# Kernel optimization log

Hardware: AMD Instinct MI355X
Metric: run time of the kernel (lower is better)

## Reference

```python
import jax, jax.numpy as jnp
import numpy as np

B, T, D, L, VOCAB = 4, 2048, 512, 3, 256


def setup_inputs() -> dict:
    key = jax.random.key(0)
    ks = jax.random.split(key, 5)
    x = jax.random.randint(ks[0], (B, T), 0, VOCAB, dtype=jnp.int32)
    embed = jax.random.normal(ks[1], (VOCAB, D), dtype=jnp.float32) * 0.02
    k = jnp.ones((L,), dtype=jnp.float32)
    ln_gamma = jnp.ones((L, D), dtype=jnp.float32)
    ln_beta = jnp.zeros((L, D), dtype=jnp.float32)
    W1 = jax.random.normal(ks[2], (L, D, 4 * D), dtype=jnp.float32) * 0.02
    b1 = jnp.zeros((L, 4 * D), dtype=jnp.float32)
    W2 = jax.random.normal(ks[3], (L, 4 * D, D), dtype=jnp.float32) * 0.02
    b2 = jnp.zeros((L, D), dtype=jnp.float32)
    return {"x": x, "embed": embed, "k": k, "ln_gamma": ln_gamma,
            "ln_beta": ln_beta, "W1": W1, "b1": b1, "W2": W2, "b2": b2}


def _layernorm(x, g, b, eps=1e-3):  # keras default eps=1e-3
    mu = jnp.mean(x, axis=-1, keepdims=True)
    var = jnp.mean(jnp.square(x - mu), axis=-1, keepdims=True)
    return (x - mu) * jax.lax.rsqrt(var + eps) * g + b


def reference(x, embed, k, ln_gamma, ln_beta, W1, b1, W2, b2):
    h = embed[x]  # (B,T,D)
    # CumprodBoundaryDimension: cumprod over feature dim, tanh, cumsum over time
    bd = jnp.cumsum(jnp.tanh(jnp.cumprod(h, axis=-1)), axis=1)
    h = h + h * bd
    t = jnp.arange(T)
    dist = jnp.abs((t[:, None] - t[None, :]).astype(jnp.float32))  # (T,T)
    causal = (t[None, :] <= t[:, None]).astype(jnp.float32)
    for l in range(L):
        # DeltaImportance
        h_cum = jnp.cumsum(h, axis=1)
        h_prev = jnp.pad(h[:, :-1, :], ((0, 0), (1, 0), (0, 0)))
        mag = jnp.linalg.norm(h_cum - h_prev, axis=-1)  # (B,T)
        decay = jnp.exp(-jax.nn.softplus(k[l]) * dist) * causal  # (T,T)
        # importance[b,i,j] = mag[b,i]*decay[i,j]; context = importance @ h
        ctx = jnp.abs(mag[:, :, None] * jnp.einsum('ij,bjd->bid', decay, h))
        y = _layernorm(ctx, ln_gamma[l], ln_beta[l])
        y = jax.nn.gelu(y @ W1[l] + b1[l], approximate=False) @ W2[l] + b2[l]
        h = h + y
    return h @ embed.T  # tied output projection (B,T,VOCAB)
```

## Files before the change

### kernel.cpp

```cpp
#include <hip/hip_runtime.h>
#include <math.h>


constexpr int Bc = 4, Tc = 2048, Dc = 512, Hc = 2048, Vc = 256;
constexpr int TSF = 16, NCF = 128, WARM = 20;

typedef __attribute__((ext_vector_type(8))) short short8;
typedef __attribute__((ext_vector_type(4))) float f32x4;

__device__ inline unsigned short f2bf(float f) {
  unsigned int u = __float_as_uint(f);
  u += 0x7fffu + ((u >> 16) & 1u);
  return (unsigned short)(u >> 16);
}

__device__ inline void gload_lds16(const void* g, void* l) {
  __builtin_amdgcn_global_load_lds(
      (const __attribute__((address_space(1))) void*)g,
      (__attribute__((address_space(3))) void*)l, 16, 0, 0);
}

__device__ inline float gelu_f(float z) {
  float x = z * 0.707106781186547524f;
  float ax = fabsf(x);
  float t = 1.0f / (1.0f + 0.3275911f * ax);
  float poly = t*(0.254829592f + t*(-0.284496736f + t*(1.421413741f +
               t*(-1.453152027f + t*1.061405429f))));
  float er = 1.0f - poly * __expf(-ax*ax);
  er = copysignf(er, x);
  return 0.5f * z * (1.0f + er);
}

__device__ inline void tr32(const float* Wl, unsigned short* Wtl,
                            int R, int C, int c0, int r0, int tid,
                            float (*tile)[33]) {
  int tx = tid & 31, ty = tid >> 5;
  for (int i = ty; i < 32; i += 8)
    tile[i][tx] = Wl[(size_t)(r0+i)*C + (c0+tx)];
  __syncthreads();
  for (int i = ty; i < 32; i += 8)
    Wtl[(size_t)(c0+i)*R + (r0+tx)] = f2bf(tile[tx][i]);
}

__global__ __launch_bounds__(256) void wprep(
    const float* __restrict__ W1, unsigned short* __restrict__ W1t,
    const float* __restrict__ W2, unsigned short* __restrict__ W2t,
    const float* __restrict__ embed, unsigned short* __restrict__ emb)
{
  __shared__ float tile[32][33];
  int bid = blockIdx.x, tid = threadIdx.x;
  if (bid < 3072) {
    int l = bid >> 10, rem = bid & 1023;
    int cx = rem & 63, ry = rem >> 6;
    tr32(W1 + (size_t)l*Dc*Hc, W1t + (size_t)l*Dc*Hc, Dc, Hc,
         cx*32, ry*32, tid, tile);
  } else if (bid < 6144) {
    int b2 = bid - 3072;
    int l = b2 >> 10, rem = b2 & 1023;
    int cx = rem & 15, ry = rem >> 4;
    tr32(W2 + (size_t)l*Hc*Dc, W2t + (size_t)l*Hc*Dc, Hc, Dc,
         cx*32, ry*32, tid, tile);
  } else {
    int i = (bid - 6144)*256 + tid;
    if (i < Vc*Dc) emb[i] = f2bf(embed[i]);
  }
}

__global__ __launch_bounds__(1024) void embed_part(
    const int* __restrict__ x, const float* __restrict__ embed,
    float* __restrict__ th, float* __restrict__ partA)
{
  int c = blockIdx.x, b = blockIdx.y;
  int wv = threadIdx.x >> 6, lane = threadIdx.x & 63;
  int token = b*Tc + c*TSF + wv;
  int row = x[token];
  const float* e = embed + (size_t)row * Dc + lane * 8;
  float v[8];
  {
    float4 a = *(const float4*)e;
    float4 bb = *(const float4*)(e + 4);
    v[0]=a.x; v[1]=a.y; v[2]=a.z; v[3]=a.w;
    v[4]=bb.x; v[5]=bb.y; v[6]=bb.z; v[7]=bb.w;
  }
  float p = v[0];
  #pragma unroll
  for (int j=1;j<8;++j) p *= v[j];
  float incl = p;
  #pragma unroll
  for (int off=1; off<64; off<<=1) {
    float t = __shfl_up(incl, off);
    if (lane >= off) incl *= t;
  }
  float excl = __shfl_up(incl, 1);
  if (lane == 0) excl = 1.0f;
  float cc = excl;
  float o[8];
  #pragma unroll
  for (int j=0;j<8;++j) { cc *= v[j]; o[j] = tanhf(cc); }
  float* dst = th + (size_t)token * Dc + lane * 8;
  *(float4*)dst     = make_float4(o[0],o[1],o[2],o[3]);
  *(float4*)(dst+4) = make_float4(o[4],o[5],o[6],o[7]);
  __syncthreads();
  int d = threadIdx.x;
  if (d < Dc) {
    const float* pp = th + ((size_t)b*Tc + c*TSF)*Dc + d;
    float s = 0.f;
    #pragma unroll
    for (int t=0;t<TSF;++t) s += pp[(size_t)t*Dc];
    partA[((size_t)b*NCF + c)*Dc + d] = s;
  }
}

__global__ __launch_bounds__(512) void part_prefix(float* __restrict__ part)
{
  int pair = blockIdx.x * 8 + (threadIdx.x >> 6);
  int lane = threadIdx.x & 63;
  int b = pair >> 9, d = pair & 511;
  size_t i0 = ((size_t)b*NCF + 2*lane)*Dc + d;
  float v0 = part[i0];
  float v1 = part[i0 + Dc];
  float ps = v0 + v1;
  float incl = ps;
  #pragma unroll
  for (int off=1; off<64; off<<=1) {
    float t = __shfl_up(incl, off);
    if (lane >= off) incl += t;
  }
  float excl = incl - ps;
  part[i0]      = excl;
  part[i0 + Dc] = excl + v0;
}

__global__ __launch_bounds__(512) void bd_apply(
    const float* __restrict__ th, const float* __restrict__ partA,
    const int* __restrict__ x, const float* __restrict__ embed,
    float* __restrict__ h, float* __restrict__ partB)
{
  int c = blockIdx.x, b = blockIdx.y, d = threadIdx.x;
  float acc = partA[((size_t)b*NCF + c)*Dc + d];
  float hsum = 0.f;
  #pragma unroll
  for (int t=0;t<TSF;++t) {
    int tt = c*TSF + t;
    size_t idx = ((size_t)b*Tc + tt)*Dc + d;
    acc += th[idx];
    int row = x[b*Tc + tt];
    float e = embed[(size_t)row*Dc + d];
    float hv = e * (1.0f + acc);
    h[idx] = hv;
    hsum += hv;
  }
  partB[((size_t)b*NCF + c)*Dc + d] = hsum;
}

__global__ __launch_bounds__(512) void mag_scan_ln(
    const float* __restrict__ h, const float* __restrict__ part,
    const float* __restrict__ kvec, int l,
    const float* __restrict__ g, const float* __restrict__ bt,
    unsigned short* __restrict__ yb)
{
  __shared__ float redA[8][TSF];
  __shared__ float redB[8][TSF];
  __shared__ float mag[TSF], muS[TSF], rsS[TSF];
  int c = blockIdx.x, b = blockIdx.y, d = threadIdx.x;
  int lane = d & 63, wv = d >> 6;
  float acc = part[((size_t)b*NCF + c)*Dc + d];
  int t0 = c * TSF;
  const float* hbase = h + (size_t)b*Tc*Dc + d;
  float hp = (t0 > 0) ? hbase[(size_t)(t0-1)*Dc] : 0.f;
  float hv[TSF];
  #pragma unroll
  for (int t=0;t<TSF;++t) {
    hv[t] = hbase[(size_t)(t0+t)*Dc];
    acc += hv[t];
    float diff = acc - hp;
    hp = hv[t];
    float s = diff * diff;
    #pragma unroll
    for (int off=32; off; off>>=1) s += __shfl_down(s, off);
    if (!lane) redA[wv][t] = s;
  }
  float kk = kvec[l];
  float sp = kk > 0.f ? kk + log1pf(expf(-kk)) : log1pf(expf(kk));
  float w = expf(-sp);
  int ts = t0 - WARM; if (ts < 0) ts = 0;
  float s = 0.f;
  for (int t=ts; t<t0; ++t) s = hbase[(size_t)t*Dc] + w*s;
  __syncthreads();
  if (d < TSF) {
    float m = 0.f;
    #pragma unroll
    for (int w2=0;w2<8;++w2) m += redA[w2][d];
    mag[d] = sqrtf(m);
  }
  __syncthreads();
  #pragma unroll
  for (int t=0;t<TSF;++t) {
    s = hv[t] + w * s;
    float cv = mag[t] * fabsf(s);
    hv[t] = cv;
    float s1 = cv, s2 = cv * cv;
    #pragma unroll
    for (int off=32; off; off>>=1) {
      s1 += __shfl_down(s1, off);
      s2 += __shfl_down(s2, off);
    }
    if (!lane) { redA[wv][t] = s1; redB[wv][t] = s2; }
  }
  __syncthreads();
  if (d < TSF) {
    float m1 = 0.f, m2 = 0.f;
    #pragma unroll
    for (int w2=0;w2<8;++w2) { m1 += redA[w2][d]; m2 += redB[w2][d]; }
    float mu = m1 * (1.f/Dc);
    float var = fmaxf(m2 * (1.f/Dc) - mu*mu, 0.f);
    muS[d] = mu;
    rsS[d] = rsqrtf(var + 1e-3f);
  }
  __syncthreads();
  float gv = g[l*Dc + d], bv = bt[l*Dc + d];
  unsigned short* yp = yb + ((size_t)b*Tc + t0)*Dc + d;
  #pragma unroll
  for (int t=0;t<TSF;++t)
    yp[(size_t)t*Dc] = f2bf((hv[t] - muS[t]) * rsS[t] * gv + bv);
}

template<int CH> __device__ inline int swz(int row) {
  if constexpr (CH == 8) return row & 7;
  else return (row & 3) ^ ((row >> 3) & 1);
}

template<int EPI, int TM, int TN, int BK>
__global__ __launch_bounds__(256) void mgemm(
    const unsigned short* __restrict__ A,
    const unsigned short* __restrict__ Bt,
    const float* __restrict__ bias,
    float* __restrict__ C, unsigned short* __restrict__ Cb,
    float* __restrict__ part,
    int N, int K, int nrow)
{
  constexpr int CH = BK / 8;
  constexpr int PA = TM*CH/256, PB = TN*CH/256;
  constexpr int WM = TM/2, WN = TN/2;
  constexpr int AM = WM/16, AN = WN/16;
  constexpr int NKH = BK/32;
  constexpr int ASTG = TM*BK, BSTG = TN*BK;
  __shared__ unsigned short As[2*ASTG];
  __shared__ unsigned short Bs[2*BSTG];
  int tid = threadIdx.x;
  int lane = tid & 63, w = tid >> 6;
  int wr = w >> 1, wc = w & 1;
  int bid = blockIdx.x;
  int xcd = bid & 7, i = bid >> 3;
  int npx = nrow >> 3;
  int m0 = (xcd * npx + (i % npx)) * TM;
  int n0 = (i / npx) * TN;

  const unsigned short* ag[PA];
  const unsigned short* bg[PB];
  int aldst[PA], bldst[PB];
  #pragma unroll
  for (int p=0;p<PA;++p) {
    int ci = p*256 + tid;
    int row = ci / CH, cp = ci % CH;
    int cg = cp ^ swz<CH>(row);
    ag[p] = A + (size_t)(m0+row)*K + cg*8;
    aldst[p] = (p*256 + w*64)*8;
  }
  #pragma unroll
  for (int p=0;p<PB;++p) {
    int ci = p*256 + tid;
    int row = ci / CH, cp = ci % CH;
    int cg = cp ^ swz<CH>(row);
    bg[p] = Bt + (size_t)(n0+row)*K + cg*8;
    bldst[p] = (p*256 + w*64)*8;
  }

  int r = lane & 15, quad = lane >> 4;
  int aoff[NKH][AM], boff[NKH][AN];
  #pragma unroll
  for (int kh=0;kh<NKH;++kh) {
    int cb = kh*4 + quad;
    #pragma unroll
    for (int i2=0;i2<AM;++i2)
      aoff[kh][i2] = (wr*WM + i2*16 + r)*BK + ((cb ^ swz<CH>(r)) & (CH-1))*8;
    #pragma unroll
    for (int j=0;j<AN;++j)
      boff[kh][j] = (wc*WN + j*16 + r)*BK + ((cb ^ swz<CH>(r)) & (CH-1))*8;
  }

  f32x4 acc[AM][AN];
  #pragma unroll
  for (int i2=0;i2<AM;++i2)
    #pragma unroll
    for (int j=0;j<AN;++j)
      acc[i2][j] = (f32x4){0.f,0.f,0.f,0.f};

  #pragma unroll
  for (int p=0;p<PA;++p) gload_lds16(ag[p], &As[aldst[p]]);
  #pragma unroll
  for (int p=0;p<PB;++p) gload_lds16(bg[p], &Bs[bldst[p]]);

  int nk = K / BK;
  for (int ki = 0; ki < nk; ++ki) {
    __syncthreads();
    int cur = ki & 1, nxt = cur ^ 1;
    if (ki + 1 < nk) {
      int kk = (ki + 1) * BK;
      #pragma unroll
      for (int p=0;p<PA;++p) gload_lds16(ag[p] + kk, &As[nxt*ASTG + aldst[p]]);
      #pragma unroll
      for (int p=0;p<PB;++p) gload_lds16(bg[p] + kk, &Bs[nxt*BSTG + bldst[p]]);
    }
    #pragma unroll
    for (int kh=0;kh<NKH;++kh) {
      short8 af[AM], bfr[AN];
      #pragma unroll
      for (int i2=0;i2<AM;++i2) af[i2] = *(const short8*)&As[cur*ASTG + aoff[kh][i2]];
      #pragma unroll
      for (int j=0;j<AN;++j) bfr[j] = *(const short8*)&Bs[cur*BSTG + boff[kh][j]];
      #pragma unroll
      for (int i2=0;i2<AM;++i2)
        #pragma unroll
        for (int j=0;j<AN;++j)
          acc[i2][j] = __builtin_amdgcn_mfma_f32_16x16x32_bf16(af[i2], bfr[j], acc[i2][j], 0, 0, 0);
    }
  }

  #pragma unroll
  for (int i2=0;i2<AM;++i2) {
    int rowb = m0 + wr*WM + i2*16 + quad*4;
    #pragma unroll
    for (int j=0;j<AN;++j) {
      int col = n0 + wc*WN + j*16 + r;
      float bv = 0.f;
      if (EPI != 2) bv = bias[col];
      float ps = 0.f;
      #pragma unroll
      for (int reg=0;reg<4;++reg) {
        size_t idx = (size_t)(rowb + reg) * N + col;
        float z = acc[i2][j][reg] + bv;
        if (EPI == 0) {
          Cb[idx] = f2bf(gelu_f(z));
        } else if (EPI == 1) {
          float hv = C[idx] + z;
          C[idx] = hv;
          ps += hv;
          if (Cb) Cb[idx] = f2bf(hv);
        } else {
          C[idx] = z;
        }
      }
      if (EPI == 1 && part) {
        ps += __shfl_xor(ps, 16);
        ps += __shfl_xor(ps, 32);
        if (quad == 0) {
          int chunk = (m0 + wr*WM + i2*16) >> 4;
          part[(size_t)chunk * N + col] = ps;
        }
      }
    }
  }
}

extern "C" void kernel_launch(void* const* d_in, const int* in_sizes, int n_in,
                              void* d_out, int out_size, void* d_ws, size_t ws_size,
                              hipStream_t stream) {
  const int*   x     = (const int*)  d_in[0];
  const float* embed = (const float*)d_in[1];
  const float* kvec  = (const float*)d_in[2];
  const float* g     = (const float*)d_in[3];
  const float* bt    = (const float*)d_in[4];
  const float* W1    = (const float*)d_in[5];
  const float* b1    = (const float*)d_in[6];
  const float* W2    = (const float*)d_in[7];
  const float* b2    = (const float*)d_in[8];
  float* out = (float*)d_out;

  const size_t NTD = (size_t)Bc * Tc * Dc;
  const size_t NTH = (size_t)Bc * Tc * Hc;
  char* wsb = (char*)d_ws;
  float* h      = (float*)wsb;                wsb += NTD*4;
  float* tmpA   = (float*)wsb;                wsb += NTD*4;
  float* partA  = (float*)wsb;                wsb += (size_t)Bc*NCF*Dc*4;
  float* partB  = (float*)wsb;                wsb += (size_t)Bc*NCF*Dc*4;
  unsigned short* yb   = (unsigned short*)wsb; wsb += NTD*2;
  unsigned short* a1b  = (unsigned short*)wsb; wsb += NTH*2;
  unsigned short* hb   = (unsigned short*)wsb; wsb += NTD*2;
  unsigned short* W1t  = (unsigned short*)wsb; wsb += (size_t)3*Dc*Hc*2;
  unsigned short* W2t  = (unsigned short*)wsb; wsb += (size_t)3*Dc*Hc*2;
  unsigned short* emb  = (unsigned short*)wsb; wsb += (size_t)Vc*Dc*2;

  wprep<<<dim3(6144 + (Vc*Dc+255)/256), 256, 0, stream>>>(
      W1, W1t, W2, W2t, embed, emb);

  embed_part<<<dim3(NCF, Bc), 1024, 0, stream>>>(x, embed, tmpA, partA);
  part_prefix<<<dim3(256), 512, 0, stream>>>(partA);
  bd_apply<<<dim3(NCF, Bc), 512, 0, stream>>>(tmpA, partA, x, embed, h, partB);
  part_prefix<<<dim3(256), 512, 0, stream>>>(partB);

  for (int l = 0; l < 3; ++l) {
    mag_scan_ln<<<dim3(NCF, Bc), 512, 0, stream>>>(h, partB, kvec, l, g, bt, yb);
    mgemm<0,64,64,64><<<dim3(128*(Hc/64)), 256, 0, stream>>>(
        yb, W1t + (size_t)l*Hc*Dc, b1 + (size_t)l*Hc, nullptr, a1b, nullptr,
        Hc, Dc, 128);
    mgemm<1,64,64,64><<<dim3(128*(Dc/64)), 256, 0, stream>>>(
        a1b, W2t + (size_t)l*Dc*Hc, b2 + (size_t)l*Dc, h,
        (l == 2) ? hb : nullptr, (l < 2) ? partB : nullptr, Dc, Hc, 128);
    if (l < 2) part_prefix<<<dim3(256), 512, 0, stream>>>(partB);
  }
  mgemm<2,64,64,32><<<dim3(128*(Vc/64)), 256, 0, stream>>>(
      hb, emb, nullptr, out, nullptr, nullptr, Vc, Dc, 128);
}
```

Before: 407.5 us.

## Fuse prologue scans and mag/LN into cooperative kernels with grid syncs

Merges the embedding cumprod/tanh, both chunk-prefix scans, the boundary apply and the first-layer mag-scan/layernorm into one cooperative kernel that uses grid-wide syncs. It also folds the per-layer part_prefix into the following mag-scan kernel. The tanh intermediate stays in shared memory instead of a global tmp buffer. This removes several kernel launches and a full-size global round trip, at the cost of cooperative launch overhead and grid barrier latency, and it needs all 512 blocks to be co-resident.

```diff
diff --git a/kernel.cpp b/kernel.cpp
--- a/kernel.cpp
+++ b/kernel.cpp
@@ -1,6 +1,9 @@
 #include <hip/hip_runtime.h>
+#include <hip/hip_cooperative_groups.h>
 #include <math.h>
 
+
+namespace cg = cooperative_groups;
 
 constexpr int Bc = 4, Tc = 2048, Dc = 512, Hc = 2048, Vc = 256;
 constexpr int TSF = 16, NCF = 128, WARM = 20;
@@ -66,55 +69,7 @@
   }
 }
 
-__global__ __launch_bounds__(1024) void embed_part(
-    const int* __restrict__ x, const float* __restrict__ embed,
-    float* __restrict__ th, float* __restrict__ partA)
-{
-  int c = blockIdx.x, b = blockIdx.y;
-  int wv = threadIdx.x >> 6, lane = threadIdx.x & 63;
-  int token = b*Tc + c*TSF + wv;
-  int row = x[token];
-  const float* e = embed + (size_t)row * Dc + lane * 8;
-  float v[8];
-  {
-    float4 a = *(const float4*)e;
-    float4 bb = *(const float4*)(e + 4);
-    v[0]=a.x; v[1]=a.y; v[2]=a.z; v[3]=a.w;
-    v[4]=bb.x; v[5]=bb.y; v[6]=bb.z; v[7]=bb.w;
-  }
-  float p = v[0];
-  #pragma unroll
-  for (int j=1;j<8;++j) p *= v[j];
-  float incl = p;
-  #pragma unroll
-  for (int off=1; off<64; off<<=1) {
-    float t = __shfl_up(incl, off);
-    if (lane >= off) incl *= t;
-  }
-  float excl = __shfl_up(incl, 1);
-  if (lane == 0) excl = 1.0f;
-  float cc = excl;
-  float o[8];
-  #pragma unroll
-  for (int j=0;j<8;++j) { cc *= v[j]; o[j] = tanhf(cc); }
-  float* dst = th + (size_t)token * Dc + lane * 8;
-  *(float4*)dst     = make_float4(o[0],o[1],o[2],o[3]);
-  *(float4*)(dst+4) = make_float4(o[4],o[5],o[6],o[7]);
-  __syncthreads();
-  int d = threadIdx.x;
-  if (d < Dc) {
-    const float* pp = th + ((size_t)b*Tc + c*TSF)*Dc + d;
-    float s = 0.f;
-    #pragma unroll
-    for (int t=0;t<TSF;++t) s += pp[(size_t)t*Dc];
-    partA[((size_t)b*NCF + c)*Dc + d] = s;
-  }
-}
-
-__global__ __launch_bounds__(512) void part_prefix(float* __restrict__ part)
-{
-  int pair = blockIdx.x * 8 + (threadIdx.x >> 6);
-  int lane = threadIdx.x & 63;
+__device__ inline void prefix_scan_pair(float* part, int pair, int lane) {
   int b = pair >> 9, d = pair & 511;
   size_t i0 = ((size_t)b*NCF + 2*lane)*Dc + d;
   float v0 = part[i0];
@@ -131,47 +86,17 @@
   part[i0 + Dc] = excl + v0;
 }
 
-__global__ __launch_bounds__(512) void bd_apply(
-    const float* __restrict__ th, const float* __restrict__ partA,
-    const int* __restrict__ x, const float* __restrict__ embed,
-    float* __restrict__ h, float* __restrict__ partB)
+__device__ inline void mag_scan_ln_body(
+    float* hv, const float* hbase, float accp, int t0, int c, int b, int d,
+    int lane, int wv, float w,
+    const float* g, const float* bt, int l, unsigned short* yb,
+    float (*redA)[TSF], float (*redB)[TSF],
+    float* mag, float* muS, float* rsS)
 {
-  int c = blockIdx.x, b = blockIdx.y, d = threadIdx.x;
-  float acc = partA[((size_t)b*NCF + c)*Dc + d];
-  float hsum = 0.f;
+  float acc = accp;
+  float hp = (t0 > 0) ? hbase[(size_t)(t0-1)*Dc] : 0.f;
   #pragma unroll
   for (int t=0;t<TSF;++t) {
-    int tt = c*TSF + t;
-    size_t idx = ((size_t)b*Tc + tt)*Dc + d;
-    acc += th[idx];
-    int row = x[b*Tc + tt];
-    float e = embed[(size_t)row*Dc + d];
-    float hv = e * (1.0f + acc);
-    h[idx] = hv;
-    hsum += hv;
-  }
-  partB[((size_t)b*NCF + c)*Dc + d] = hsum;
-}
-
-__global__ __launch_bounds__(512) void mag_scan_ln(
-    const float* __restrict__ h, const float* __restrict__ part,
-    const float* __restrict__ kvec, int l,
-    const float* __restrict__ g, const float* __restrict__ bt,
-    unsigned short* __restrict__ yb)
-{
-  __shared__ float redA[8][TSF];
-  __shared__ float redB[8][TSF];
-  __shared__ float mag[TSF], muS[TSF], rsS[TSF];
-  int c = blockIdx.x, b = blockIdx.y, d = threadIdx.x;
-  int lane = d & 63, wv = d >> 6;
-  float acc = part[((size_t)b*NCF + c)*Dc + d];
-  int t0 = c * TSF;
-  const float* hbase = h + (size_t)b*Tc*Dc + d;
-  float hp = (t0 > 0) ? hbase[(size_t)(t0-1)*Dc] : 0.f;
-  float hv[TSF];
-  #pragma unroll
-  for (int t=0;t<TSF;++t) {
-    hv[t] = hbase[(size_t)(t0+t)*Dc];
     acc += hv[t];
     float diff = acc - hp;
     hp = hv[t];
@@ -180,9 +105,6 @@
     for (int off=32; off; off>>=1) s += __shfl_down(s, off);
     if (!lane) redA[wv][t] = s;
   }
-  float kk = kvec[l];
-  float sp = kk > 0.f ? kk + log1pf(expf(-kk)) : log1pf(expf(kk));
-  float w = expf(-sp);
   int ts = t0 - WARM; if (ts < 0) ts = 0;
   float s = 0.f;
   for (int t=ts; t<t0; ++t) s = hbase[(size_t)t*Dc] + w*s;
@@ -223,6 +145,122 @@
   #pragma unroll
   for (int t=0;t<TSF;++t)
     yp[(size_t)t*Dc] = f2bf((hv[t] - muS[t]) * rsS[t] * gv + bv);
+}
+
+__device__ inline float decay_w(const float* kvec, int l) {
+  float kk = kvec[l];
+  float sp = kk > 0.f ? kk + log1pf(expf(-kk)) : log1pf(expf(kk));
+  return expf(-sp);
+}
+
+__global__ __launch_bounds__(512, 4) void coop_prologue(
+    const int* __restrict__ x, const float* __restrict__ embed,
+    float* __restrict__ partA, float* __restrict__ partB,
+    float* __restrict__ h, const float* __restrict__ kvec,
+    const float* __restrict__ g, const float* __restrict__ bt,
+    unsigned short* __restrict__ yb)
+{
+  cg::grid_group gg = cg::this_grid();
+  __shared__ float thL[TSF][Dc];
+  __shared__ float redA[8][TSF], redB[8][TSF];
+  __shared__ float mag[TSF], muS[TSF], rsS[TSF];
+  int c = blockIdx.x, b = blockIdx.y;
+  int tid = threadIdx.x, wv = tid >> 6, lane = tid & 63;
+
+  #pragma unroll
+  for (int rep=0; rep<2; ++rep) {
+    int tk = wv + rep*8;
+    int token = b*Tc + c*TSF + tk;
+    int row = x[token];
+    const float* e = embed + (size_t)row * Dc + lane * 8;
+    float v[8];
+    {
+      float4 a = *(const float4*)e;
+      float4 bb = *(const float4*)(e + 4);
+      v[0]=a.x; v[1]=a.y; v[2]=a.z; v[3]=a.w;
+      v[4]=bb.x; v[5]=bb.y; v[6]=bb.z; v[7]=bb.w;
+    }
+    float p = v[0];
+    #pragma unroll
+    for (int j=1;j<8;++j) p *= v[j];
+    float incl = p;
+    #pragma unroll
+    for (int off=1; off<64; off<<=1) {
+      float t = __shfl_up(incl, off);
+      if (lane >= off) incl *= t;
+    }
+    float excl = __shfl_up(incl, 1);
+    if (lane == 0) excl = 1.0f;
+    float cc = excl;
+    #pragma unroll
+    for (int j=0;j<8;++j) { cc *= v[j]; thL[tk][lane*8+j] = tanhf(cc); }
+  }
+  __syncthreads();
+  int d = tid;
+  {
+    float s = 0.f;
+    #pragma unroll
+    for (int t=0;t<TSF;++t) s += thL[t][d];
+    partA[((size_t)b*NCF + c)*Dc + d] = s;
+  }
+  __threadfence();
+  gg.sync();
+  int gw = (b*NCF + c)*8 + wv;
+  if (gw < 2048) prefix_scan_pair(partA, gw, lane);
+  __threadfence();
+  gg.sync();
+  float hv[TSF];
+  {
+    float acc = partA[((size_t)b*NCF + c)*Dc + d];
+    float hsum = 0.f;
+    #pragma unroll
+    for (int t=0;t<TSF;++t) {
+      int tt = c*TSF + t;
+      acc += thL[t][d];
+      int row = x[b*Tc + tt];
+      float e = embed[(size_t)row*Dc + d];
+      hv[t] = e * (1.0f + acc);
+      h[((size_t)b*Tc + tt)*Dc + d] = hv[t];
+      hsum += hv[t];
+    }
+    partB[((size_t)b*NCF + c)*Dc + d] = hsum;
+  }
+  __threadfence();
+  gg.sync();
+  if (gw < 2048) prefix_scan_pair(partB, gw, lane);
+  __threadfence();
+  gg.sync();
+  float w = decay_w(kvec, 0);
+  float accp = partB[((size_t)b*NCF + c)*Dc + d];
+  const float* hbase = h + (size_t)b*Tc*Dc + d;
+  mag_scan_ln_body(hv, hbase, accp, c*TSF, c, b, d, lane, wv, w,
+                   g, bt, 0, yb, redA, redB, mag, muS, rsS);
+}
+
+__global__ __launch_bounds__(512, 4) void coop_magscan(
+    float* __restrict__ partB, const float* __restrict__ h,
+    const float* __restrict__ kvec, int l,
+    const float* __restrict__ g, const float* __restrict__ bt,
+    unsigned short* __restrict__ yb)
+{
+  cg::grid_group gg = cg::this_grid();
+  __shared__ float redA[8][TSF], redB[8][TSF];
+  __shared__ float mag[TSF], muS[TSF], rsS[TSF];
+  int c = blockIdx.x, b = blockIdx.y;
+  int tid = threadIdx.x, wv = tid >> 6, lane = tid & 63;
+  int gw = (b*NCF + c)*8 + wv;
+  if (gw < 2048) prefix_scan_pair(partB, gw, lane);
+  __threadfence();
+  gg.sync();
+  int d = tid, t0 = c*TSF;
+  const float* hbase = h + (size_t)b*Tc*Dc + d;
+  float hv[TSF];
+  #pragma unroll
+  for (int t=0;t<TSF;++t) hv[t] = hbase[(size_t)(t0+t)*Dc];
+  float w = decay_w(kvec, l);
+  float accp = partB[((size_t)b*NCF + c)*Dc + d];
+  mag_scan_ln_body(hv, hbase, accp, t0, c, b, d, lane, wv, w,
+                   g, bt, l, yb, redA, redB, mag, muS, rsS);
 }
 
 template<int CH> __device__ inline int swz(int row) {
@@ -381,7 +419,6 @@
   const size_t NTH = (size_t)Bc * Tc * Hc;
   char* wsb = (char*)d_ws;
   float* h      = (float*)wsb;                wsb += NTD*4;
-  float* tmpA   = (float*)wsb;                wsb += NTD*4;
   float* partA  = (float*)wsb;                wsb += (size_t)Bc*NCF*Dc*4;
   float* partB  = (float*)wsb;                wsb += (size_t)Bc*NCF*Dc*4;
   unsigned short* yb   = (unsigned short*)wsb; wsb += NTD*2;
@@ -394,20 +431,28 @@
   wprep<<<dim3(6144 + (Vc*Dc+255)/256), 256, 0, stream>>>(
       W1, W1t, W2, W2t, embed, emb);
 
-  embed_part<<<dim3(NCF, Bc), 1024, 0, stream>>>(x, embed, tmpA, partA);
-  part_prefix<<<dim3(256), 512, 0, stream>>>(partA);
-  bd_apply<<<dim3(NCF, Bc), 512, 0, stream>>>(tmpA, partA, x, embed, h, partB);
-  part_prefix<<<dim3(256), 512, 0, stream>>>(partB);
+  {
+    void* args[] = { (void*)&x, (void*)&embed, (void*)&partA, (void*)&partB,
+                     (void*)&h, (void*)&kvec, (void*)&g, (void*)&bt,
+                     (void*)&yb };
+    hipLaunchCooperativeKernel((void*)coop_prologue, dim3(NCF, Bc),
+                               dim3(512), args, 0, stream);
+  }
 
   for (int l = 0; l < 3; ++l) {
-    mag_scan_ln<<<dim3(NCF, Bc), 512, 0, stream>>>(h, partB, kvec, l, g, bt, yb);
+    if (l > 0) {
+      int ll = l;
+      void* args[] = { (void*)&partB, (void*)&h, (void*)&kvec, (void*)&ll,
+                       (void*)&g, (void*)&bt, (void*)&yb };
+      hipLaunchCooperativeKernel((void*)coop_magscan, dim3(NCF, Bc),
+                                 dim3(512), args, 0, stream);
+    }
     mgemm<0,64,64,64><<<dim3(128*(Hc/64)), 256, 0, stream>>>(
         yb, W1t + (size_t)l*Hc*Dc, b1 + (size_t)l*Hc, nullptr, a1b, nullptr,
         Hc, Dc, 128);
     mgemm<1,64,64,64><<<dim3(128*(Dc/64)), 256, 0, stream>>>(
         a1b, W2t + (size_t)l*Dc*Hc, b2 + (size_t)l*Dc, h,
         (l == 2) ? hb : nullptr, (l < 2) ? partB : nullptr, Dc, Hc, 128);
-    if (l < 2) part_prefix<<<dim3(256), 512, 0, stream>>>(partB);
   }
   mgemm<2,64,64,32><<<dim3(128*(Vc/64)), 256, 0, stream>>>(
       hb, emb, nullptr, out, nullptr, nullptr, Vc, Dc, 128);
```

After: 1.281 ms. +214.4%, slower.
